# Performance work log

Hardware: AMD Instinct MI355X
Metric: run time of the kernel (lower is better)

Reference implementation:

```python
import jax, jax.numpy as jnp
import numpy as np

B, N, S, D1, D2 = 8, 8192, 2048, 128, 256
MLP = [256, 128]
IN_CH = D1 + D2
EPS_INTERP = 1e-8
EPS_BN = 1e-5


def setup_inputs() -> dict:
    key = jax.random.key(0)
    ks = jax.random.split(key, 12)
    inp = {
        "xyz1": jax.random.normal(ks[0], (B, 3, N), dtype=jnp.float32),
        "xyz2": jax.random.normal(ks[1], (B, 3, S), dtype=jnp.float32),
        "points1": jax.random.normal(ks[2], (B, D1, N), dtype=jnp.float32),
        "points2": jax.random.normal(ks[3], (B, D2, S), dtype=jnp.float32),
    }
    # Conv1d(k=1) weights are [out, in]; BN has gamma/beta per channel.
    last = IN_CH
    for i, oc in enumerate(MLP):
        inp[f"W{i}"] = jax.random.normal(ks[4 + 2 * i], (oc, last), dtype=jnp.float32) * (1.0 / np.sqrt(last))
        inp[f"b{i}"] = jnp.zeros((oc,), dtype=jnp.float32)
        inp[f"g{i}"] = jnp.ones((oc,), dtype=jnp.float32)
        inp[f"be{i}"] = jnp.zeros((oc,), dtype=jnp.float32)
        last = oc
    return inp


def _interpolate(xyz1, xyz2, points2):
    # xyz1: [B,3,N] -> [B,N,3]; xyz2: [B,3,S] -> [B,S,3]; points2: [B,D2,S] -> [B,S,D2]
    x1 = jnp.transpose(xyz1, (0, 2, 1))
    x2 = jnp.transpose(xyz2, (0, 2, 1))
    p2 = jnp.transpose(points2, (0, 2, 1))
    # squared distances [B,N,S]
    dists = (jnp.sum(x1 * x1, -1)[:, :, None]
             - 2.0 * jnp.einsum("bnc,bsc->bns", x1, x2)
             + jnp.sum(x2 * x2, -1)[:, None, :])
    neg_d, idx = jax.lax.top_k(-dists, 3)         # 3 nearest neighbors
    d = -neg_d                                     # [B,N,3]
    recip = 1.0 / (d + EPS_INTERP)
    weight = recip / jnp.sum(recip, axis=2, keepdims=True)
    gathered = jax.vmap(lambda p, i: p[i])(p2, idx)   # [B,N,3,D2]
    return jnp.sum(gathered * weight[..., None], axis=2)  # [B,N,D2]


def _conv_bn_relu(x, W, b, g, be):
    # x: [B,C,N]; 1x1 conv == channel GEMM
    y = jnp.einsum("oc,bcn->bon", W, x) + b[None, :, None]
    mean = jnp.mean(y, axis=(0, 2), keepdims=True)
    var = jnp.mean((y - mean) ** 2, axis=(0, 2), keepdims=True)  # biased, torch BN train
    y = (y - mean) * jax.lax.rsqrt(var + EPS_BN)
    y = y * g[None, :, None] + be[None, :, None]
    return jax.nn.relu(y)


def reference(xyz1, xyz2, points1, points2, W0, b0, g0, be0, W1, b1, g1, be1):
    interp = _interpolate(xyz1, xyz2, points2)               # [B,N,D2]
    p1 = jnp.transpose(points1, (0, 2, 1))                    # [B,N,D1]
    new_points = jnp.concatenate([p1, interp], axis=-1)       # [B,N,D1+D2]
    new_points = jnp.transpose(new_points, (0, 2, 1))         # [B,D1+D2,N]
    new_points = _conv_bn_relu(new_points, W0, b0, g0, be0)
    new_points = _conv_bn_relu(new_points, W1, b1, g1, be1)
    return new_points
```

## Files before the change

### kernel.cpp

```cpp
#include <hip/hip_runtime.h>

typedef unsigned short ushort_t;
typedef __bf16 bf16x8 __attribute__((ext_vector_type(8)));
typedef float floatx4 __attribute__((ext_vector_type(4)));

#define B_ 8
#define N_ 8192
#define S_ 2048
#define D1_ 128
#define D2_ 256
#define INCH_ 384
#define M_ 65536

#define ASYNC_CP16(g, l)                                                  \
  __builtin_amdgcn_global_load_lds(                                       \
      (const __attribute__((address_space(1))) void*)(g),                 \
      (__attribute__((address_space(3))) void*)(l), 16, 0, 0)

constexpr size_t OFF_STATS = 0;
constexpr size_t OFF_W0B   = 8192;
constexpr size_t OFF_W1B   = 204800;
constexpr size_t OFF_X2P   = 270336;
constexpr size_t OFF_P2T   = 532480;
constexpr size_t OFF_XC    = 8921088;
constexpr size_t OFF_Y1    = 59252736;
constexpr size_t OFF_PS0   = OFF_P2T;
constexpr size_t OFF_PQ0   = OFF_P2T + 524288;
constexpr size_t OFF_PS1   = OFF_P2T + 1048576;
constexpr size_t OFF_PQ1   = OFF_P2T + 1572864;

__device__ __forceinline__ ushort_t f2bf(float f) {
  __bf16 h = (__bf16)f;
  union { __bf16 h; ushort_t u; } v;
  v.h = h;
  return v.u;
}
__device__ __forceinline__ float bf2f(ushort_t h) {
  return __uint_as_float(((unsigned int)h) << 16);
}

__device__ __forceinline__ void ins3(float e, int s,
                                     float& c0, float& c1, float& c2,
                                     int& i0, int& i1, int& i2) {
  bool l0 = e < c0, l1 = e < c1, l2 = e < c2;
  float nf0 = fminf(e, c0);
  float nf1 = __builtin_amdgcn_fmed3f(e, c0, c1);
  float nf2 = __builtin_amdgcn_fmed3f(e, c1, c2);
  i2 = l1 ? i1 : (l2 ? s : i2);
  i1 = l0 ? i0 : (l1 ? s : i1);
  i0 = l0 ? s : i0;
  c0 = nf0; c1 = nf1; c2 = nf2;
}

__global__ __launch_bounds__(256) void k_prep(const float* __restrict__ W0,
                                              const float* __restrict__ W1,
                                              const float* __restrict__ xyz2,
                                              ushort_t* __restrict__ W0b,
                                              ushort_t* __restrict__ W1b,
                                              float4* __restrict__ x2p) {
  int i = blockIdx.x * 256 + threadIdx.x;
  if (i < 98304) {
    W0b[i] = f2bf(W0[i]);
  } else if (i < 131072) {
    W1b[i - 98304] = f2bf(W1[i - 98304]);
  } else {
    int idx = i - 131072;
    int b = idx >> 11, s = idx & (S_ - 1);
    const float* base = xyz2 + (size_t)b * 3 * S_;
    float x = base[s], y = base[S_ + s], z = base[2 * S_ + s];
    x2p[idx] = make_float4(x, y, z, 0.5f * (x * x + y * y + z * z));
  }
}

__global__ void k_tr_p2(const float* __restrict__ P2, ushort_t* __restrict__ p2t) {
  __shared__ float t[32][33];
  int b = blockIdx.z;
  int s0 = blockIdx.x * 32;
  int c0 = blockIdx.y * 32;
  int tx = threadIdx.x, ty = threadIdx.y;
#pragma unroll
  for (int j = 0; j < 4; j++) {
    int c = c0 + ty + j * 8;
    t[ty + j * 8][tx] = P2[((size_t)b * D2_ + c) * S_ + s0 + tx];
  }
  __syncthreads();
#pragma unroll
  for (int j = 0; j < 4; j++) {
    int s = s0 + ty + j * 8;
    p2t[((size_t)b * S_ + s) * D2_ + c0 + tx] = f2bf(t[tx][ty + j * 8]);
  }
}

__global__ void k_tr_p1(const float* __restrict__ P1, ushort_t* __restrict__ Xc) {
  __shared__ float t[32][33];
  int b = blockIdx.z;
  int n0 = blockIdx.x * 32;
  int c0 = blockIdx.y * 32;
  int tx = threadIdx.x, ty = threadIdx.y;
#pragma unroll
  for (int j = 0; j < 4; j++) {
    int c = c0 + ty + j * 8;
    t[ty + j * 8][tx] = P1[((size_t)b * D1_ + c) * N_ + n0 + tx];
  }
  __syncthreads();
#pragma unroll
  for (int j = 0; j < 4; j++) {
    int n = n0 + ty + j * 8;
    Xc[((size_t)b * N_ + n) * INCH_ + c0 + tx] = f2bf(t[tx][ty + j * 8]);
  }
}

__global__ __launch_bounds__(512, 8) void k_knn(const float* __restrict__ xyz1,
                                                const float4* __restrict__ x2p,
                                                const ushort_t* __restrict__ p2t,
                                                ushort_t* __restrict__ Xc) {
  __shared__ float4 xs[8 * 289];
  __shared__ float wsh[64 * 3];
  __shared__ int   ish[64 * 3];
  int t = threadIdx.x;
  int q0 = blockIdx.x * 64;
  int b = q0 >> 13;
  int n0 = q0 & (N_ - 1);
  for (int l = t; l < S_; l += 512)
    xs[(l >> 8) * 289 + (l & 255)] = x2p[(size_t)b * S_ + l];
  int sub = t & 7;
  int qg = t >> 3;
  int n = n0 + qg;
  float qx = xyz1[((size_t)b * 3 + 0) * N_ + n];
  float qy = xyz1[((size_t)b * 3 + 1) * N_ + n];
  float qz = xyz1[((size_t)b * 3 + 2) * N_ + n];
  float nrm1 = qx * qx + qy * qy + qz * qz;
  __syncthreads();
  const float4* bp = xs + sub * 289;
  float k0 = 3e38f, k1 = 3e38f, k2 = 3e38f, k3 = 3e38f;
#pragma unroll 4
  for (int i = 0; i < 256; ++i) {
    float4 P = bp[i];
    float e = fmaf(-qx, P.x, fmaf(-qy, P.y, fmaf(-qz, P.z, P.w)));
    float dd = fmaf(2.f, e, nrm1);
    unsigned int kb = (__float_as_uint(dd) & 0xFFFFFF00u) | (unsigned int)i;
    float k = __uint_as_float(kb);
    float n0_ = fminf(k, k0);
    float n1_ = __builtin_amdgcn_fmed3f(k, k0, k1);
    float n2_ = __builtin_amdgcn_fmed3f(k, k1, k2);
    float n3_ = __builtin_amdgcn_fmed3f(k, k2, k3);
    k0 = n0_; k1 = n1_; k2 = n2_; k3 = n3_;
  }
  float ed[4];
  int   si[4];
  {
    float kk[4] = {k0, k1, k2, k3};
#pragma unroll
    for (int c = 0; c < 4; ++c) {
      int loc = (int)(__float_as_uint(kk[c]) & 255u);
      float4 P = bp[loc];
      float e = fmaf(-qx, P.x, fmaf(-qy, P.y, fmaf(-qz, P.z, P.w)));
      ed[c] = fmaf(2.f, e, nrm1);
      si[c] = (sub << 8) + loc;
    }
  }
  float c0 = 3e38f, c1 = 3e38f, c2 = 3e38f;
  int i0 = 0, i1 = 0, i2 = 0;
#pragma unroll
  for (int c = 0; c < 4; ++c) ins3(ed[c], si[c], c0, c1, c2, i0, i1, i2);
#pragma unroll
  for (int d = 1; d < 8; d <<= 1) {
    float e0 = __shfl_xor(c0, d); int s0 = __shfl_xor(i0, d);
    float e1 = __shfl_xor(c1, d); int s1 = __shfl_xor(i1, d);
    float e2 = __shfl_xor(c2, d); int s2 = __shfl_xor(i2, d);
    ins3(e0, s0, c0, c1, c2, i0, i1, i2);
    ins3(e1, s1, c0, c1, c2, i0, i1, i2);
    ins3(e2, s2, c0, c1, c2, i0, i1, i2);
  }
  if (sub == 0) {
    float r0 = 1.f / (c0 + 1e-8f);
    float r1 = 1.f / (c1 + 1e-8f);
    float r2 = 1.f / (c2 + 1e-8f);
    float rs = 1.f / (r0 + r1 + r2);
    wsh[qg * 3 + 0] = r0 * rs; wsh[qg * 3 + 1] = r1 * rs; wsh[qg * 3 + 2] = r2 * rs;
    ish[qg * 3 + 0] = i0; ish[qg * 3 + 1] = i1; ish[qg * 3 + 2] = i2;
  }
  __syncthreads();
  int lane = t & 63, grp = t >> 6;
  size_t sbase2 = (size_t)b * S_;
#pragma unroll 2
  for (int it = 0; it < 8; ++it) {
    int ql = it * 8 + grp;
    int q = q0 + ql;
    float w0 = wsh[ql * 3 + 0], w1 = wsh[ql * 3 + 1], w2 = wsh[ql * 3 + 2];
    int j0 = ish[ql * 3 + 0], j1 = ish[ql * 3 + 1], j2 = ish[ql * 3 + 2];
    ushort4 a0 = *(const ushort4*)&p2t[(sbase2 + j0) * D2_ + lane * 4];
    ushort4 a1 = *(const ushort4*)&p2t[(sbase2 + j1) * D2_ + lane * 4];
    ushort4 a2 = *(const ushort4*)&p2t[(sbase2 + j2) * D2_ + lane * 4];
    ushort4 o;
    o.x = f2bf(w0 * bf2f(a0.x) + w1 * bf2f(a1.x) + w2 * bf2f(a2.x));
    o.y = f2bf(w0 * bf2f(a0.y) + w1 * bf2f(a1.y) + w2 * bf2f(a2.y));
    o.z = f2bf(w0 * bf2f(a0.z) + w1 * bf2f(a1.z) + w2 * bf2f(a2.z));
    o.w = f2bf(w0 * bf2f(a0.w) + w1 * bf2f(a1.w) + w2 * bf2f(a2.w));
    *(ushort4*)&Xc[(size_t)q * INCH_ + D1_ + lane * 4] = o;
  }
}

__global__ __launch_bounds__(256) void k_redstats(const float* __restrict__ ps,
                                                  const float* __restrict__ pq,
                                                  float* __restrict__ sum,
                                                  float* __restrict__ ssq,
                                                  int ncols, int nrows) {
  __shared__ float ls[4], lq[4];
  int col = blockIdx.x;
  int t = threadIdx.x;
  float s = 0.f, q = 0.f;
  for (int r = t; r < nrows; r += 256) {
    s += ps[(size_t)r * ncols + col];
    q += pq[(size_t)r * ncols + col];
  }
#pragma unroll
  for (int d = 1; d < 64; d <<= 1) {
    s += __shfl_xor(s, d);
    q += __shfl_xor(q, d);
  }
  if ((t & 63) == 0) { ls[t >> 6] = s; lq[t >> 6] = q; }
  __syncthreads();
  if (t == 0) {
    sum[col] = ls[0] + ls[1] + ls[2] + ls[3];
    ssq[col] = lq[0] + lq[1] + lq[2] + lq[3];
  }
}

__global__ __launch_bounds__(512) void k_gemm1(const ushort_t* __restrict__ A,
                                               const ushort_t* __restrict__ Bw,
                                               ushort_t* __restrict__ Cc,
                                               float* __restrict__ psum,
                                               float* __restrict__ pssq) {
  __shared__ __align__(16) ushort_t As[128 * 32];
  __shared__ __align__(16) ushort_t Bs[256 * 32];
  __shared__ float red_s[2][256], red_q[2][256];
  const int tid = threadIdx.x;
  const int m0 = blockIdx.x * 128;
  const int wave = tid >> 6;
  const int wuni = __builtin_amdgcn_readfirstlane(wave);
  const int lane = tid & 63;
  const int quad = lane >> 4;
  const int l16 = lane & 15;
  const int wrow = (wave >> 2) * 64;
  const int wcol = (wave & 3) * 64;
  const int arow = tid >> 2, aseg = tid & 3;
  floatx4 acc[4][4];
#pragma unroll
  for (int i = 0; i < 4; i++)
#pragma unroll
    for (int j = 0; j < 4; j++) acc[i][j] = (floatx4){0.f, 0.f, 0.f, 0.f};

  for (int k0 = 0; k0 < INCH_; k0 += 32) {
    ASYNC_CP16(&A[(size_t)(m0 + arow) * INCH_ + k0 + aseg * 8], &As[wuni * 512]);
#pragma unroll
    for (int it = 0; it < 2; it++) {
      int l = tid + it * 512;
      int row = l >> 2, seg = l & 3;
      ASYNC_CP16(&Bw[(size_t)row * INCH_ + k0 + seg * 8], &Bs[it * 4096 + wuni * 512]);
    }
    __syncthreads();
    bf16x8 af[4], bfr[4];
#pragma unroll
    for (int mt = 0; mt < 4; mt++) af[mt] = *(const bf16x8*)&As[(wrow + mt * 16 + l16) * 32 + quad * 8];
#pragma unroll
    for (int nt = 0; nt < 4; nt++) bfr[nt] = *(const bf16x8*)&Bs[(wcol + nt * 16 + l16) * 32 + quad * 8];
#pragma unroll
    for (int mt = 0; mt < 4; mt++)
#pragma unroll
      for (int nt = 0; nt < 4; nt++)
        acc[mt][nt] = __builtin_amdgcn_mfma_f32_16x16x32_bf16(af[mt], bfr[nt], acc[mt][nt], 0, 0, 0);
    __syncthreads();
  }
#pragma unroll
  for (int mt = 0; mt < 4; mt++) {
#pragma unroll
    for (int i = 0; i < 4; i++) {
      int row = m0 + wrow + mt * 16 + quad * 4 + i;
#pragma unroll
      for (int nt = 0; nt < 4; nt++) {
        int col = wcol + nt * 16 + l16;
        Cc[(size_t)row * 256 + col] = f2bf(acc[mt][nt][i]);
      }
    }
  }
#pragma unroll
  for (int nt = 0; nt < 4; nt++) {
    float s = 0.f, s2 = 0.f;
#pragma unroll
    for (int mt = 0; mt < 4; mt++)
#pragma unroll
      for (int i = 0; i < 4; i++) {
        float v = acc[mt][nt][i];
        s += v;
        s2 = fmaf(v, v, s2);
      }
    s += __shfl_xor(s, 16);  s2 += __shfl_xor(s2, 16);
    s += __shfl_xor(s, 32);  s2 += __shfl_xor(s2, 32);
    if (quad == 0) {
      int col = wcol + nt * 16 + l16;
      red_s[wave >> 2][col] = s;
      red_q[wave >> 2][col] = s2;
    }
  }
  __syncthreads();
  if (tid < 256) {
    psum[(size_t)blockIdx.x * 256 + tid] = red_s[0][tid] + red_s[1][tid];
    pssq[(size_t)blockIdx.x * 256 + tid] = red_q[0][tid] + red_q[1][tid];
  }
}

__global__ __launch_bounds__(256, 4) void k_gemm2t(const ushort_t* __restrict__ Y1,
                                                   const ushort_t* __restrict__ Bw,
                                                   const float* __restrict__ sum0,
                                                   const float* __restrict__ ssq0,
                                                   const float* __restrict__ g0,
                                                   const float* __restrict__ be0,
                                                   ushort_t* __restrict__ Y2t,
                                                   float* __restrict__ psum,
                                                   float* __restrict__ pssq) {
  __shared__ __align__(16) char ubuf[64 * 129 * 4];
  __shared__ float scs[256], shs[256];
  __shared__ float red_s[2][128], red_q[2][128];
  ushort_t* As = (ushort_t*)ubuf;
  ushort_t* Bs = (ushort_t*)(ubuf + 4096);
  float* tb = (float*)ubuf;
  const int tid = threadIdx.x;
  const int m0 = blockIdx.x * 64;
  const int b = m0 >> 13;
  const int n0 = m0 & (N_ - 1);
  const int wave = tid >> 6;
  const int wuni = __builtin_amdgcn_readfirstlane(wave);
  const int lane = tid & 63;
  const int quad = lane >> 4;
  const int l16 = lane & 15;
  const int wrow = (wave >> 1) * 32;
  const int wcol = (wave & 1) * 64;
  {
    float mean = sum0[tid] * (1.f / 65536.f);
    float var = ssq0[tid] * (1.f / 65536.f) - mean * mean;
    float sc = rsqrtf(var + 1e-5f) * g0[tid];
    scs[tid] = sc;
    shs[tid] = be0[tid] - mean * sc;
  }
  floatx4 acc[2][4];
#pragma unroll
  for (int i = 0; i < 2; i++)
#pragma unroll
    for (int j = 0; j < 4; j++) acc[i][j] = (floatx4){0.f, 0.f, 0.f, 0.f};
  __syncthreads();

  const int arow = tid >> 2, aseg = tid & 3;
  for (int k0 = 0; k0 < 256; k0 += 32) {
#pragma unroll
    for (int it = 0; it < 2; it++) {
      int l = tid + it * 256;
      int row = l >> 2, seg = l & 3;
      ASYNC_CP16(&Bw[(size_t)row * 256 + k0 + seg * 8], &Bs[it * 2048 + wuni * 512]);
    }
    {
      ushort4 y01 = *(const ushort4*)&Y1[(size_t)(m0 + arow) * 256 + k0 + aseg * 8];
      ushort4 y23 = *(const ushort4*)&Y1[(size_t)(m0 + arow) * 256 + k0 + aseg * 8 + 4];
      int c = k0 + aseg * 8;
      ushort4 o0, o1;
      o0.x = f2bf(fmaxf(fmaf(bf2f(y01.x), scs[c + 0], shs[c + 0]), 0.f));
      o0.y = f2bf(fmaxf(fmaf(bf2f(y01.y), scs[c + 1], shs[c + 1]), 0.f));
      o0.z = f2bf(fmaxf(fmaf(bf2f(y01.z), scs[c + 2], shs[c + 2]), 0.f));
      o0.w = f2bf(fmaxf(fmaf(bf2f(y01.w), scs[c + 3], shs[c + 3]), 0.f));
      o1.x = f2bf(fmaxf(fmaf(bf2f(y23.x), scs[c + 4], shs[c + 4]), 0.f));
      o1.y = f2bf(fmaxf(fmaf(bf2f(y23.y), scs[c + 5], shs[c + 5]), 0.f));
      o1.z = f2bf(fmaxf(fmaf(bf2f(y23.z), scs[c + 6], shs[c + 6]), 0.f));
      o1.w = f2bf(fmaxf(fmaf(bf2f(y23.w), scs[c + 7], shs[c + 7]), 0.f));
      *(ushort4*)&As[arow * 32 + aseg * 8] = o0;
      *(ushort4*)&As[arow * 32 + aseg * 8 + 4] = o1;
    }
    __syncthreads();
    bf16x8 af[2], bfr[4];
#pragma unroll
    for (int mt = 0; mt < 2; mt++) af[mt] = *(const bf16x8*)&As[(wrow + mt * 16 + l16) * 32 + quad * 8];
#pragma unroll
    for (int nt = 0; nt < 4; nt++) bfr[nt] = *(const bf16x8*)&Bs[(wcol + nt * 16 + l16) * 32 + quad * 8];
#pragma unroll
    for (int mt = 0; mt < 2; mt++)
#pragma unroll
      for (int nt = 0; nt < 4; nt++)
        acc[mt][nt] = __builtin_amdgcn_mfma_f32_16x16x32_bf16(af[mt], bfr[nt], acc[mt][nt], 0, 0, 0);
    __syncthreads();
  }
#pragma unroll
  for (int nt = 0; nt < 4; nt++) {
    float s = 0.f, s2 = 0.f;
#pragma unroll
    for (int mt = 0; mt < 2; mt++)
#pragma unroll
      for (int i = 0; i < 4; i++) {
        float v = acc[mt][nt][i];
        s += v;
        s2 = fmaf(v, v, s2);
      }
    s += __shfl_xor(s, 16);  s2 += __shfl_xor(s2, 16);
    s += __shfl_xor(s, 32);  s2 += __shfl_xor(s2, 32);
    if (quad == 0) {
      int col = wcol + nt * 16 + l16;
      red_s[wave >> 1][col] = s;
      red_q[wave >> 1][col] = s2;
    }
  }
#pragma unroll
  for (int mt = 0; mt < 2; mt++)
#pragma unroll
    for (int i = 0; i < 4; i++) {
      int rl = wrow + mt * 16 + quad * 4 + i;
#pragma unroll
      for (int nt = 0; nt < 4; nt++) {
        int col = wcol + nt * 16 + l16;
        tb[rl * 129 + col] = acc[mt][nt][i];
      }
    }
  __syncthreads();
  if (tid < 128) {
    psum[(size_t)blockIdx.x * 128 + tid] = red_s[0][tid] + red_s[1][tid];
    pssq[(size_t)blockIdx.x * 128 + tid] = red_q[0][tid] + red_q[1][tid];
  }
#pragma unroll
  for (int it = 0; it < 8; ++it) {
    int idx = it * 256 + tid;
    int c = idx >> 4;
    int j4 = (idx & 15) * 4;
    ushort4 v;
    v.x = f2bf(tb[(j4 + 0) * 129 + c]);
    v.y = f2bf(tb[(j4 + 1) * 129 + c]);
    v.z = f2bf(tb[(j4 + 2) * 129 + c]);
    v.w = f2bf(tb[(j4 + 3) * 129 + c]);
    *(ushort4*)&Y2t[((size_t)(b * 128 + c)) * N_ + n0 + j4] = v;
  }
}

__global__ __launch_bounds__(256) void k_out2(const ushort_t* __restrict__ Y2t,
                                              const float* __restrict__ sum1,
                                              const float* __restrict__ ssq1,
                                              const float* __restrict__ g1,
                                              const float* __restrict__ be1,
                                              float* __restrict__ out) {
  __shared__ float sc1[128], sh1[128];
  int tid = threadIdx.x;
  if (tid < 128) {
    float mean = sum1[tid] * (1.f / 65536.f);
    float var = ssq1[tid] * (1.f / 65536.f) - mean * mean;
    float sc = rsqrtf(var + 1e-5f) * g1[tid];
    sc1[tid] = sc;
    sh1[tid] = be1[tid] - mean * sc;
  }
  __syncthreads();
#pragma unroll
  for (int it = 0; it < 4; ++it) {
    int fid = (it * 2048 + blockIdx.x) * 256 + tid;
    int r = fid >> 11;
    int c = r & 127;
    int n4 = (fid & 2047) * 4;
    ushort4 y = *(const ushort4*)&Y2t[((size_t)r << 13) + n4];
    float sc = sc1[c], sh = sh1[c];
    float4 v;
    v.x = fmaxf(fmaf(bf2f(y.x), sc, sh), 0.f);
    v.y = fmaxf(fmaf(bf2f(y.y), sc, sh), 0.f);
    v.z = fmaxf(fmaf(bf2f(y.z), sc, sh), 0.f);
    v.w = fmaxf(fmaf(bf2f(y.w), sc, sh), 0.f);
    *(float4*)&out[((size_t)r << 13) + n4] = v;
  }
}

extern "C" void kernel_launch(void* const* d_in, const int* in_sizes, int n_in,
                              void* d_out, int out_size, void* d_ws, size_t ws_size,
                              hipStream_t stream) {
  const float* xyz1    = (const float*)d_in[0];
  const float* xyz2    = (const float*)d_in[1];
  const float* points1 = (const float*)d_in[2];
  const float* points2 = (const float*)d_in[3];
  const float* W0 = (const float*)d_in[4];
  const float* g0 = (const float*)d_in[6];
  const float* be0 = (const float*)d_in[7];
  const float* W1 = (const float*)d_in[8];
  const float* g1 = (const float*)d_in[10];
  const float* be1 = (const float*)d_in[11];
  float* out = (float*)d_out;
  char* ws = (char*)d_ws;

  float* sum0   = (float*)(ws + OFF_STATS);
  float* ssq0   = sum0 + 256;
  float* sum1   = sum0 + 512;
  float* ssq1   = sum0 + 640;
  ushort_t* W0b = (ushort_t*)(ws + OFF_W0B);
  ushort_t* W1b = (ushort_t*)(ws + OFF_W1B);
  float4* x2p   = (float4*)(ws + OFF_X2P);
  ushort_t* p2t = (ushort_t*)(ws + OFF_P2T);
  ushort_t* Xc  = (ushort_t*)(ws + OFF_XC);
  ushort_t* Y1b = (ushort_t*)(ws + OFF_Y1);
  ushort_t* Y2t = (ushort_t*)(ws + OFF_XC);
  float* psum0  = (float*)(ws + OFF_PS0);
  float* pssq0  = (float*)(ws + OFF_PQ0);
  float* psum1  = (float*)(ws + OFF_PS1);
  float* pssq1  = (float*)(ws + OFF_PQ1);

  k_prep<<<576, 256, 0, stream>>>(W0, W1, xyz2, W0b, W1b, x2p);
  k_tr_p2<<<dim3(64, 8, 8), dim3(32, 8), 0, stream>>>(points2, p2t);
  k_tr_p1<<<dim3(256, 4, 8), dim3(32, 8), 0, stream>>>(points1, Xc);
  k_knn<<<1024, 512, 0, stream>>>(xyz1, x2p, p2t, Xc);
  k_gemm1<<<512, 512, 0, stream>>>(Xc, W0b, Y1b, psum0, pssq0);
  k_redstats<<<256, 256, 0, stream>>>(psum0, pssq0, sum0, ssq0, 256, 512);
  k_gemm2t<<<1024, 256, 0, stream>>>(Y1b, W1b, sum0, ssq0, g0, be0,
                                     Y2t, psum1, pssq1);
  k_redstats<<<128, 256, 0, stream>>>(psum1, pssq1, sum1, ssq1, 128, 1024);
  k_out2<<<2048, 256, 0, stream>>>(Y2t, sum1, ssq1, g1, be1, out);
}
```

Before: 217.3 us.

## Merge prep/transpose kernels and pack kNN candidates for packed-FP32 math

Fuses the weight-cast, xyz2 packing, and both points transposes into one launch, so two kernel launches and their gaps go away. Separately, the kNN kernel now stores candidate coordinates in LDS as interleaved pairs (x0,x1,y0,y1,...), so two distances can be computed with 2-wide vector float ops (packed FMA on CDNA). This roughly halves the distance arithmetic per candidate, while the top-4 insertion cost stays the same. The changed LDS layout also changes the bank access pattern, and the fused launch branches on block index, which could cause some divergence between the two block types.

```diff
diff --git a/kernel.cpp b/kernel.cpp
--- a/kernel.cpp
+++ b/kernel.cpp
@@ -3,6 +3,7 @@
 typedef unsigned short ushort_t;
 typedef __bf16 bf16x8 __attribute__((ext_vector_type(8)));
 typedef float floatx4 __attribute__((ext_vector_type(4)));
+typedef float floatx2 __attribute__((ext_vector_type(2)));
 
 #define B_ 8
 #define N_ 8192
@@ -52,61 +53,76 @@
   c0 = nf0; c1 = nf1; c2 = nf2;
 }
 
-__global__ __launch_bounds__(256) void k_prep(const float* __restrict__ W0,
-                                              const float* __restrict__ W1,
-                                              const float* __restrict__ xyz2,
-                                              ushort_t* __restrict__ W0b,
-                                              ushort_t* __restrict__ W1b,
-                                              float4* __restrict__ x2p) {
-  int i = blockIdx.x * 256 + threadIdx.x;
-  if (i < 98304) {
-    W0b[i] = f2bf(W0[i]);
-  } else if (i < 131072) {
-    W1b[i - 98304] = f2bf(W1[i - 98304]);
+__device__ __forceinline__ void ins4(float k, float& k0, float& k1,
+                                     float& k2, float& k3) {
+  float n0 = fminf(k, k0);
+  float n1 = __builtin_amdgcn_fmed3f(k, k0, k1);
+  float n2 = __builtin_amdgcn_fmed3f(k, k1, k2);
+  float n3 = __builtin_amdgcn_fmed3f(k, k2, k3);
+  k0 = n0; k1 = n1; k2 = n2; k3 = n3;
+}
+
+__global__ __launch_bounds__(256) void k_pre(const float* __restrict__ W0,
+                                             const float* __restrict__ W1,
+                                             const float* __restrict__ xyz2,
+                                             const float* __restrict__ P2,
+                                             const float* __restrict__ P1,
+                                             ushort_t* __restrict__ W0b,
+                                             ushort_t* __restrict__ W1b,
+                                             float4* __restrict__ x2p,
+                                             ushort_t* __restrict__ p2t,
+                                             ushort_t* __restrict__ Xc) {
+  __shared__ float t[32][33];
+  const int blk = blockIdx.x;
+  const int tid = threadIdx.x;
+  if (blk < 576) {
+    int i = blk * 256 + tid;
+    if (i < 98304) {
+      W0b[i] = f2bf(W0[i]);
+    } else if (i < 131072) {
+      W1b[i - 98304] = f2bf(W1[i - 98304]);
+    } else {
+      int idx = i - 131072;
+      int b = idx >> 11, s = idx & (S_ - 1);
+      const float* base = xyz2 + (size_t)b * 3 * S_;
+      float x = base[s], y = base[S_ + s], z = base[2 * S_ + s];
+      x2p[idx] = make_float4(x, y, z, 0.5f * (x * x + y * y + z * z));
+    }
+    return;
+  }
+  int tx = tid & 31, ty = tid >> 5;
+  if (blk < 4672) {
+    int idx = blk - 576;
+    int s0 = (idx & 63) * 32;
+    int c0 = ((idx >> 6) & 7) * 32;
+    int b = idx >> 9;
+#pragma unroll
+    for (int j = 0; j < 4; j++) {
+      int c = c0 + ty + j * 8;
+      t[ty + j * 8][tx] = P2[((size_t)b * D2_ + c) * S_ + s0 + tx];
+    }
+    __syncthreads();
+#pragma unroll
+    for (int j = 0; j < 4; j++) {
+      int s = s0 + ty + j * 8;
+      p2t[((size_t)b * S_ + s) * D2_ + c0 + tx] = f2bf(t[tx][ty + j * 8]);
+    }
   } else {
-    int idx = i - 131072;
-    int b = idx >> 11, s = idx & (S_ - 1);
-    const float* base = xyz2 + (size_t)b * 3 * S_;
-    float x = base[s], y = base[S_ + s], z = base[2 * S_ + s];
-    x2p[idx] = make_float4(x, y, z, 0.5f * (x * x + y * y + z * z));
-  }
-}
-
-__global__ void k_tr_p2(const float* __restrict__ P2, ushort_t* __restrict__ p2t) {
-  __shared__ float t[32][33];
-  int b = blockIdx.z;
-  int s0 = blockIdx.x * 32;
-  int c0 = blockIdx.y * 32;
-  int tx = threadIdx.x, ty = threadIdx.y;
-#pragma unroll
-  for (int j = 0; j < 4; j++) {
-    int c = c0 + ty + j * 8;
-    t[ty + j * 8][tx] = P2[((size_t)b * D2_ + c) * S_ + s0 + tx];
-  }
-  __syncthreads();
-#pragma unroll
-  for (int j = 0; j < 4; j++) {
-    int s = s0 + ty + j * 8;
-    p2t[((size_t)b * S_ + s) * D2_ + c0 + tx] = f2bf(t[tx][ty + j * 8]);
-  }
-}
-
-__global__ void k_tr_p1(const float* __restrict__ P1, ushort_t* __restrict__ Xc) {
-  __shared__ float t[32][33];
-  int b = blockIdx.z;
-  int n0 = blockIdx.x * 32;
-  int c0 = blockIdx.y * 32;
-  int tx = threadIdx.x, ty = threadIdx.y;
-#pragma unroll
-  for (int j = 0; j < 4; j++) {
-    int c = c0 + ty + j * 8;
-    t[ty + j * 8][tx] = P1[((size_t)b * D1_ + c) * N_ + n0 + tx];
-  }
-  __syncthreads();
-#pragma unroll
-  for (int j = 0; j < 4; j++) {
-    int n = n0 + ty + j * 8;
-    Xc[((size_t)b * N_ + n) * INCH_ + c0 + tx] = f2bf(t[tx][ty + j * 8]);
+    int idx = blk - 4672;
+    int n0 = (idx & 255) * 32;
+    int c0 = ((idx >> 8) & 3) * 32;
+    int b = idx >> 10;
+#pragma unroll
+    for (int j = 0; j < 4; j++) {
+      int c = c0 + ty + j * 8;
+      t[ty + j * 8][tx] = P1[((size_t)b * D1_ + c) * N_ + n0 + tx];
+    }
+    __syncthreads();
+#pragma unroll
+    for (int j = 0; j < 4; j++) {
+      int n = n0 + ty + j * 8;
+      Xc[((size_t)b * N_ + n) * INCH_ + c0 + tx] = f2bf(t[tx][ty + j * 8]);
+    }
   }
 }
 
@@ -114,15 +130,21 @@
                                                 const float4* __restrict__ x2p,
                                                 const ushort_t* __restrict__ p2t,
                                                 ushort_t* __restrict__ Xc) {
-  __shared__ float4 xs[8 * 289];
+  __shared__ float xs[8 * 1028];
   __shared__ float wsh[64 * 3];
   __shared__ int   ish[64 * 3];
   int t = threadIdx.x;
   int q0 = blockIdx.x * 64;
   int b = q0 >> 13;
   int n0 = q0 & (N_ - 1);
-  for (int l = t; l < S_; l += 512)
-    xs[(l >> 8) * 289 + (l & 255)] = x2p[(size_t)b * S_ + l];
+  for (int pr = t; pr < 1024; pr += 512) {
+    int ch = pr >> 7, pl = pr & 127;
+    float4 p0 = x2p[(size_t)b * S_ + 2 * pr];
+    float4 p1 = x2p[(size_t)b * S_ + 2 * pr + 1];
+    float* dst = xs + ch * 1028 + pl * 8;
+    *(floatx4*)dst       = (floatx4){p0.x, p1.x, p0.y, p1.y};
+    *(floatx4*)(dst + 4) = (floatx4){p0.z, p1.z, p0.w, p1.w};
+  }
   int sub = t & 7;
   int qg = t >> 3;
   int n = n0 + qg;
@@ -131,20 +153,23 @@
   float qz = xyz1[((size_t)b * 3 + 2) * N_ + n];
   float nrm1 = qx * qx + qy * qy + qz * qz;
   __syncthreads();
-  const float4* bp = xs + sub * 289;
+  const float* bp = xs + sub * 1028;
+  floatx2 qx2 = {qx, qx}, qy2 = {qy, qy}, qz2 = {qz, qz}, nr2 = {nrm1, nrm1};
   float k0 = 3e38f, k1 = 3e38f, k2 = 3e38f, k3 = 3e38f;
 #pragma unroll 4
-  for (int i = 0; i < 256; ++i) {
-    float4 P = bp[i];
-    float e = fmaf(-qx, P.x, fmaf(-qy, P.y, fmaf(-qz, P.z, P.w)));
-    float dd = fmaf(2.f, e, nrm1);
-    unsigned int kb = (__float_as_uint(dd) & 0xFFFFFF00u) | (unsigned int)i;
-    float k = __uint_as_float(kb);
-    float n0_ = fminf(k, k0);
-    float n1_ = __builtin_amdgcn_fmed3f(k, k0, k1);
-    float n2_ = __builtin_amdgcn_fmed3f(k, k1, k2);
-    float n3_ = __builtin_amdgcn_fmed3f(k, k2, k3);
-    k0 = n0_; k1 = n1_; k2 = n2_; k3 = n3_;
+  for (int i = 0; i < 128; ++i) {
+    floatx4 a = *(const floatx4*)&bp[i * 8];
+    floatx4 c = *(const floatx4*)&bp[i * 8 + 4];
+    floatx2 X = {a.x, a.y}, Y = {a.z, a.w};
+    floatx2 Z = {c.x, c.y}, W = {c.z, c.w};
+    floatx2 e = W - qz2 * Z;
+    e = e - qy2 * Y;
+    e = e - qx2 * X;
+    floatx2 dd = e * 2.0f + nr2;
+    unsigned kb0 = (__float_as_uint(dd.x) & 0xFFFFFF00u) | (unsigned)(2 * i);
+    unsigned kb1 = (__float_as_uint(dd.y) & 0xFFFFFF00u) | (unsigned)(2 * i + 1);
+    ins4(__uint_as_float(kb0), k0, k1, k2, k3);
+    ins4(__uint_as_float(kb1), k0, k1, k2, k3);
   }
   float ed[4];
   int   si[4];
@@ -153,8 +178,12 @@
 #pragma unroll
     for (int c = 0; c < 4; ++c) {
       int loc = (int)(__float_as_uint(kk[c]) & 255u);
-      float4 P = bp[loc];
-      float e = fmaf(-qx, P.x, fmaf(-qy, P.y, fmaf(-qz, P.z, P.w)));
+      int pair = loc >> 1, h = loc & 1;
+      float x = bp[pair * 8 + h];
+      float y = bp[pair * 8 + 2 + h];
+      float z = bp[pair * 8 + 4 + h];
+      float w = bp[pair * 8 + 6 + h];
+      float e = fmaf(-qx, x, fmaf(-qy, y, fmaf(-qz, z, w)));
       ed[c] = fmaf(2.f, e, nrm1);
       si[c] = (sub << 8) + loc;
     }
@@ -501,9 +530,8 @@
   float* psum1  = (float*)(ws + OFF_PS1);
   float* pssq1  = (float*)(ws + OFF_PQ1);
 
-  k_prep<<<576, 256, 0, stream>>>(W0, W1, xyz2, W0b, W1b, x2p);
-  k_tr_p2<<<dim3(64, 8, 8), dim3(32, 8), 0, stream>>>(points2, p2t);
-  k_tr_p1<<<dim3(256, 4, 8), dim3(32, 8), 0, stream>>>(points1, Xc);
+  k_pre<<<12864, 256, 0, stream>>>(W0, W1, xyz2, points2, points1,
+                                   W0b, W1b, x2p, p2t, Xc);
   k_knn<<<1024, 512, 0, stream>>>(xyz1, x2p, p2t, Xc);
   k_gemm1<<<512, 512, 0, stream>>>(Xc, W0b, Y1b, psum0, pssq0);
   k_redstats<<<256, 256, 0, stream>>>(psum0, pssq0, sum0, ssq0, 256, 512);
```

Measured after the change: 219.3 us. No clear change (+0.9%).

## Merge prep/transpose kernels into one launch and retile gemm1 to 64-row blocks

Applied to the files above, without the earlier changes.

Folds the weight conversion, xyz2 packing and both points transposes into one kernel dispatched by block index, removing two launches. gemm1 moves from 128-row tiles with 512 threads to 64-row tiles with 256 threads and 4 waves each covering 32x128, doubling the grid to 1024 blocks so occupancy and load balance across CUs improve. The per-block partial stats buffers double in count, so the workspace offsets and the reduction row count change to match. Smaller M tiles mean each block reloads the full weight tile per k-step, which raises LDS and global traffic for B.

```diff
diff --git a/kernel.cpp b/kernel.cpp
--- a/kernel.cpp
+++ b/kernel.cpp
@@ -25,9 +25,9 @@
 constexpr size_t OFF_XC    = 8921088;
 constexpr size_t OFF_Y1    = 59252736;
 constexpr size_t OFF_PS0   = OFF_P2T;
-constexpr size_t OFF_PQ0   = OFF_P2T + 524288;
-constexpr size_t OFF_PS1   = OFF_P2T + 1048576;
-constexpr size_t OFF_PQ1   = OFF_P2T + 1572864;
+constexpr size_t OFF_PQ0   = OFF_P2T + 1048576;
+constexpr size_t OFF_PS1   = OFF_P2T + 2097152;
+constexpr size_t OFF_PQ1   = OFF_P2T + 2621440;
 
 __device__ __forceinline__ ushort_t f2bf(float f) {
   __bf16 h = (__bf16)f;
@@ -52,61 +52,67 @@
   c0 = nf0; c1 = nf1; c2 = nf2;
 }
 
-__global__ __launch_bounds__(256) void k_prep(const float* __restrict__ W0,
-                                              const float* __restrict__ W1,
-                                              const float* __restrict__ xyz2,
-                                              ushort_t* __restrict__ W0b,
-                                              ushort_t* __restrict__ W1b,
-                                              float4* __restrict__ x2p) {
-  int i = blockIdx.x * 256 + threadIdx.x;
-  if (i < 98304) {
-    W0b[i] = f2bf(W0[i]);
-  } else if (i < 131072) {
-    W1b[i - 98304] = f2bf(W1[i - 98304]);
+__global__ __launch_bounds__(256) void k_pre(const float* __restrict__ W0,
+                                             const float* __restrict__ W1,
+                                             const float* __restrict__ xyz2,
+                                             const float* __restrict__ P2,
+                                             const float* __restrict__ P1,
+                                             ushort_t* __restrict__ W0b,
+                                             ushort_t* __restrict__ W1b,
+                                             float4* __restrict__ x2p,
+                                             ushort_t* __restrict__ p2t,
+                                             ushort_t* __restrict__ Xc) {
+  __shared__ float t[32][33];
+  const int blk = blockIdx.x;
+  const int tid = threadIdx.x;
+  if (blk < 576) {
+    int i = blk * 256 + tid;
+    if (i < 98304) {
+      W0b[i] = f2bf(W0[i]);
+    } else if (i < 131072) {
+      W1b[i - 98304] = f2bf(W1[i - 98304]);
+    } else {
+      int idx = i - 131072;
+      int b = idx >> 11, s = idx & (S_ - 1);
+      const float* base = xyz2 + (size_t)b * 3 * S_;
+      float x = base[s], y = base[S_ + s], z = base[2 * S_ + s];
+      x2p[idx] = make_float4(x, y, z, 0.5f * (x * x + y * y + z * z));
+    }
+    return;
+  }
+  int tx = tid & 31, ty = tid >> 5;
+  if (blk < 4672) {
+    int idx = blk - 576;
+    int s0 = (idx & 63) * 32;
+    int c0 = ((idx >> 6) & 7) * 32;
+    int b = idx >> 9;
+#pragma unroll
+    for (int j = 0; j < 4; j++) {
+      int c = c0 + ty + j * 8;
+      t[ty + j * 8][tx] = P2[((size_t)b * D2_ + c) * S_ + s0 + tx];
+    }
+    __syncthreads();
+#pragma unroll
+    for (int j = 0; j < 4; j++) {
+      int s = s0 + ty + j * 8;
+      p2t[((size_t)b * S_ + s) * D2_ + c0 + tx] = f2bf(t[tx][ty + j * 8]);
+    }
   } else {
-    int idx = i - 131072;
-    int b = idx >> 11, s = idx & (S_ - 1);
-    const float* base = xyz2 + (size_t)b * 3 * S_;
-    float x = base[s], y = base[S_ + s], z = base[2 * S_ + s];
-    x2p[idx] = make_float4(x, y, z, 0.5f * (x * x + y * y + z * z));
-  }
-}
-
-__global__ void k_tr_p2(const float* __restrict__ P2, ushort_t* __restrict__ p2t) {
-  __shared__ float t[32][33];
-  int b = blockIdx.z;
-  int s0 = blockIdx.x * 32;
-  int c0 = blockIdx.y * 32;
-  int tx = threadIdx.x, ty = threadIdx.y;
-#pragma unroll
-  for (int j = 0; j < 4; j++) {
-    int c = c0 + ty + j * 8;
-    t[ty + j * 8][tx] = P2[((size_t)b * D2_ + c) * S_ + s0 + tx];
-  }
-  __syncthreads();
-#pragma unroll
-  for (int j = 0; j < 4; j++) {
-    int s = s0 + ty + j * 8;
-    p2t[((size_t)b * S_ + s) * D2_ + c0 + tx] = f2bf(t[tx][ty + j * 8]);
-  }
-}
-
-__global__ void k_tr_p1(const float* __restrict__ P1, ushort_t* __restrict__ Xc) {
-  __shared__ float t[32][33];
-  int b = blockIdx.z;
-  int n0 = blockIdx.x * 32;
-  int c0 = blockIdx.y * 32;
-  int tx = threadIdx.x, ty = threadIdx.y;
-#pragma unroll
-  for (int j = 0; j < 4; j++) {
-    int c = c0 + ty + j * 8;
-    t[ty + j * 8][tx] = P1[((size_t)b * D1_ + c) * N_ + n0 + tx];
-  }
-  __syncthreads();
-#pragma unroll
-  for (int j = 0; j < 4; j++) {
-    int n = n0 + ty + j * 8;
-    Xc[((size_t)b * N_ + n) * INCH_ + c0 + tx] = f2bf(t[tx][ty + j * 8]);
+    int idx = blk - 4672;
+    int n0 = (idx & 255) * 32;
+    int c0 = ((idx >> 8) & 3) * 32;
+    int b = idx >> 10;
+#pragma unroll
+    for (int j = 0; j < 4; j++) {
+      int c = c0 + ty + j * 8;
+      t[ty + j * 8][tx] = P1[((size_t)b * D1_ + c) * N_ + n0 + tx];
+    }
+    __syncthreads();
+#pragma unroll
+    for (int j = 0; j < 4; j++) {
+      int n = n0 + ty + j * 8;
+      Xc[((size_t)b * N_ + n) * INCH_ + c0 + tx] = f2bf(t[tx][ty + j * 8]);
+    }
   }
 }
 
@@ -227,68 +233,76 @@
   }
 }
 
-__global__ __launch_bounds__(512) void k_gemm1(const ushort_t* __restrict__ A,
-                                               const ushort_t* __restrict__ Bw,
-                                               ushort_t* __restrict__ Cc,
-                                               float* __restrict__ psum,
-                                               float* __restrict__ pssq) {
-  __shared__ __align__(16) ushort_t As[128 * 32];
+__global__ __launch_bounds__(256, 4) void k_gemm1(const ushort_t* __restrict__ A,
+                                                  const ushort_t* __restrict__ Bw,
+                                                  ushort_t* __restrict__ Cc,
+                                                  float* __restrict__ psum,
+                                                  float* __restrict__ pssq) {
+  __shared__ __align__(16) ushort_t As[64 * 32];
   __shared__ __align__(16) ushort_t Bs[256 * 32];
   __shared__ float red_s[2][256], red_q[2][256];
   const int tid = threadIdx.x;
-  const int m0 = blockIdx.x * 128;
+  const int m0 = blockIdx.x * 64;
   const int wave = tid >> 6;
   const int wuni = __builtin_amdgcn_readfirstlane(wave);
   const int lane = tid & 63;
   const int quad = lane >> 4;
   const int l16 = lane & 15;
-  const int wrow = (wave >> 2) * 64;
-  const int wcol = (wave & 3) * 64;
+  const int wrow = (wave >> 1) * 32;
+  const int wcol = (wave & 1) * 128;
   const int arow = tid >> 2, aseg = tid & 3;
-  floatx4 acc[4][4];
-#pragma unroll
-  for (int i = 0; i < 4; i++)
-#pragma unroll
-    for (int j = 0; j < 4; j++) acc[i][j] = (floatx4){0.f, 0.f, 0.f, 0.f};
+  floatx4 acc[2][8];
+#pragma unroll
+  for (int i = 0; i < 2; i++)
+#pragma unroll
+    for (int j = 0; j < 8; j++) acc[i][j] = (floatx4){0.f, 0.f, 0.f, 0.f};
 
   for (int k0 = 0; k0 < INCH_; k0 += 32) {
     ASYNC_CP16(&A[(size_t)(m0 + arow) * INCH_ + k0 + aseg * 8], &As[wuni * 512]);
 #pragma unroll
-    for (int it = 0; it < 2; it++) {
-      int l = tid + it * 512;
+    for (int it = 0; it < 4; it++) {
+      int l = tid + it * 256;
       int row = l >> 2, seg = l & 3;
-      ASYNC_CP16(&Bw[(size_t)row * INCH_ + k0 + seg * 8], &Bs[it * 4096 + wuni * 512]);
+      ASYNC_CP16(&Bw[(size_t)row * INCH_ + k0 + seg * 8], &Bs[it * 2048 + wuni * 512]);
     }
     __syncthreads();
-    bf16x8 af[4], bfr[4];
-#pragma unroll
-    for (int mt = 0; mt < 4; mt++) af[mt] = *(const bf16x8*)&As[(wrow + mt * 16 + l16) * 32 + quad * 8];
-#pragma unroll
-    for (int nt = 0; nt < 4; nt++) bfr[nt] = *(const bf16x8*)&Bs[(wcol + nt * 16 + l16) * 32 + quad * 8];
-#pragma unroll
-    for (int mt = 0; mt < 4; mt++)
-#pragma unroll
-      for (int nt = 0; nt < 4; nt++)
-        acc[mt][nt] = __builtin_amdgcn_mfma_f32_16x16x32_bf16(af[mt], bfr[nt], acc[mt][nt], 0, 0, 0);
+    bf16x8 af[2];
+#pragma unroll
+    for (int mt = 0; mt < 2; mt++) af[mt] = *(const bf16x8*)&As[(wrow + mt * 16 + l16) * 32 + quad * 8];
+#pragma unroll
+    for (int half = 0; half < 2; half++) {
+      bf16x8 bfr[4];
+#pragma unroll
+      for (int j = 0; j < 4; j++) {
+        int nt = half * 4 + j;
+        bfr[j] = *(const bf16x8*)&Bs[(wcol + nt * 16 + l16) * 32 + quad * 8];
+      }
+#pragma unroll
+      for (int mt = 0; mt < 2; mt++)
+#pragma unroll
+        for (int j = 0; j < 4; j++)
+          acc[mt][half * 4 + j] =
+              __builtin_amdgcn_mfma_f32_16x16x32_bf16(af[mt], bfr[j], acc[mt][half * 4 + j], 0, 0, 0);
+    }
     __syncthreads();
   }
 #pragma unroll
-  for (int mt = 0; mt < 4; mt++) {
+  for (int mt = 0; mt < 2; mt++) {
 #pragma unroll
     for (int i = 0; i < 4; i++) {
       int row = m0 + wrow + mt * 16 + quad * 4 + i;
 #pragma unroll
-      for (int nt = 0; nt < 4; nt++) {
+      for (int nt = 0; nt < 8; nt++) {
         int col = wcol + nt * 16 + l16;
         Cc[(size_t)row * 256 + col] = f2bf(acc[mt][nt][i]);
       }
     }
   }
 #pragma unroll
-  for (int nt = 0; nt < 4; nt++) {
+  for (int nt = 0; nt < 8; nt++) {
     float s = 0.f, s2 = 0.f;
 #pragma unroll
-    for (int mt = 0; mt < 4; mt++)
+    for (int mt = 0; mt < 2; mt++)
 #pragma unroll
       for (int i = 0; i < 4; i++) {
         float v = acc[mt][nt][i];
@@ -299,12 +313,12 @@
     s += __shfl_xor(s, 32);  s2 += __shfl_xor(s2, 32);
     if (quad == 0) {
       int col = wcol + nt * 16 + l16;
-      red_s[wave >> 2][col] = s;
-      red_q[wave >> 2][col] = s2;
-    }
-  }
-  __syncthreads();
-  if (tid < 256) {
+      red_s[wave >> 1][col] = s;
+      red_q[wave >> 1][col] = s2;
+    }
+  }
+  __syncthreads();
+  {
     psum[(size_t)blockIdx.x * 256 + tid] = red_s[0][tid] + red_s[1][tid];
     pssq[(size_t)blockIdx.x * 256 + tid] = red_q[0][tid] + red_q[1][tid];
   }
@@ -501,12 +515,11 @@
   float* psum1  = (float*)(ws + OFF_PS1);
   float* pssq1  = (float*)(ws + OFF_PQ1);
 
-  k_prep<<<576, 256, 0, stream>>>(W0, W1, xyz2, W0b, W1b, x2p);
-  k_tr_p2<<<dim3(64, 8, 8), dim3(32, 8), 0, stream>>>(points2, p2t);
-  k_tr_p1<<<dim3(256, 4, 8), dim3(32, 8), 0, stream>>>(points1, Xc);
+  k_pre<<<12864, 256, 0, stream>>>(W0, W1, xyz2, points2, points1,
+                                   W0b, W1b, x2p, p2t, Xc);
   k_knn<<<1024, 512, 0, stream>>>(xyz1, x2p, p2t, Xc);
-  k_gemm1<<<512, 512, 0, stream>>>(Xc, W0b, Y1b, psum0, pssq0);
-  k_redstats<<<256, 256, 0, stream>>>(psum0, pssq0, sum0, ssq0, 256, 512);
+  k_gemm1<<<1024, 256, 0, stream>>>(Xc, W0b, Y1b, psum0, pssq0);
+  k_redstats<<<256, 256, 0, stream>>>(psum0, pssq0, sum0, ssq0, 256, 1024);
   k_gemm2t<<<1024, 256, 0, stream>>>(Y1b, W1b, sum0, ssq0, g0, be0,
                                      Y2t, psum1, pssq1);
   k_redstats<<<128, 256, 0, stream>>>(psum1, pssq1, sum1, ssq1, 128, 1024);
```

Result: no change. 219.6 us (+1.1%).
